# Optimization experiments

Hardware: AMD Instinct MI355X
Metric: run time of the kernel (lower is better)

## Reference

```python
import jax, jax.numpy as jnp
import numpy as np

B, C, H, W = 16, 5, 512, 512


def setup_inputs() -> dict:
    key = jax.random.key(0)
    k1, k2 = jax.random.split(key)
    y_pred = jax.random.normal(k1, (B, C, H, W), dtype=jnp.float32)
    y_true = jax.random.randint(k2, (B, H, W), 0, C, dtype=jnp.int64)
    return {"y_pred": y_pred, "y_true": y_true}


def reference(y_pred, y_true):
    # softmax over class dim
    probs = jax.nn.softmax(y_pred, axis=1)  # (B, C, H, W)
    # adjacent-class differences: diff[k-1] = p[k] - p[k-1], k = 1..C-1
    diff = probs[:, 1:] - probs[:, :-1]  # (B, C-1, H, W)
    c = y_pred.shape[1]
    k = jnp.arange(1, c).reshape(1, c - 1, 1, 1)  # class index k of diff
    t = y_true[:, None, :, :]  # true class per pixel
    # for k <= t: relu(p[k-1]-p[k]) = relu(-diff); for k > t: relu(diff)
    pen = jnp.where(k <= t, jax.nn.relu(-diff), jax.nn.relu(diff))
    # sum over k per pixel, then mean over all B*H*W pixels
    total = pen.sum()
    n_pix = y_pred.shape[0] * y_pred.shape[2] * y_pred.shape[3]
    return total / n_pix
```

## Files before the change

kernel.cpp:

```cpp
#include <hip/hip_runtime.h>

constexpr int Bn   = 16;
constexpr int Cn   = 5;
constexpr int HW   = 512 * 512;
constexpr int HW4  = HW / 4;
constexpr int NVEC = Bn * HW / 4;
constexpr int NBLK = 2048;
constexpr float SCALE = 1.0f / (float)(Bn * HW);

__device__ __forceinline__ float block_reduce_256(float v) {
    #pragma unroll
    for (int off = 32; off > 0; off >>= 1)
        v += __shfl_down(v, off, 64);
    __shared__ float s[4];
    const int lane = threadIdx.x & 63;
    const int wid  = threadIdx.x >> 6;
    if (lane == 0) s[wid] = v;
    __syncthreads();
    if (threadIdx.x == 0) v = (s[0] + s[1]) + (s[2] + s[3]);
    return v;
}

__device__ __forceinline__ float pixel_pen(float l0, float l1, float l2, float l3,
                                           float l4, int t) {
    float m  = fmaxf(fmaxf(fmaxf(l0, l1), fmaxf(l2, l3)), l4);
    float e0 = __expf(l0 - m);
    float e1 = __expf(l1 - m);
    float e2 = __expf(l2 - m);
    float e3 = __expf(l3 - m);
    float e4 = __expf(l4 - m);
    float S  = ((e0 + e1) + (e2 + e3)) + e4;
    float d1 = e1 - e0;
    float d2 = e2 - e1;
    float d3 = e3 - e2;
    float d4 = e4 - e3;
    float pen = 0.0f;
    pen += (t >= 1) ? fmaxf(-d1, 0.0f) : fmaxf(d1, 0.0f);
    pen += (t >= 2) ? fmaxf(-d2, 0.0f) : fmaxf(d2, 0.0f);
    pen += (t >= 3) ? fmaxf(-d3, 0.0f) : fmaxf(d3, 0.0f);
    pen += (t >= 4) ? fmaxf(-d4, 0.0f) : fmaxf(d4, 0.0f);
    return pen / S;
}

__global__ void __launch_bounds__(256)
o2_loss_partial(const float4* __restrict__ pred,
                const int4*  __restrict__ lab,
                float* __restrict__ partial) {
    float acc = 0.0f;
    const int stride = gridDim.x * 256;
    for (int v = blockIdx.x * 256 + threadIdx.x; v < NVEC; v += stride) {
        const int b   = v >> 16;
        const int hw4 = v & (HW4 - 1);
        const float4* base = pred + (size_t)b * (Cn * HW4) + hw4;
        float4 x0 = base[0 * HW4];
        float4 x1 = base[1 * HW4];
        float4 x2 = base[2 * HW4];
        float4 x3 = base[3 * HW4];
        float4 x4 = base[4 * HW4];
        int4   t  = lab[v];
        acc += pixel_pen(x0.x, x1.x, x2.x, x3.x, x4.x, t.x);
        acc += pixel_pen(x0.y, x1.y, x2.y, x3.y, x4.y, t.y);
        acc += pixel_pen(x0.z, x1.z, x2.z, x3.z, x4.z, t.z);
        acc += pixel_pen(x0.w, x1.w, x2.w, x3.w, x4.w, t.w);
    }
    acc = block_reduce_256(acc);
    if (threadIdx.x == 0) partial[blockIdx.x] = acc;
}

__global__ void __launch_bounds__(256)
o2_loss_finalize(const float* __restrict__ partial, float* __restrict__ out) {
    float v = 0.0f;
    for (int i = threadIdx.x; i < NBLK; i += 256)
        v += partial[i];
    v = block_reduce_256(v);
    if (threadIdx.x == 0) out[0] = v * SCALE;
}

extern "C" void kernel_launch(void* const* d_in, const int* in_sizes, int n_in,
                              void* d_out, int out_size, void* d_ws, size_t ws_size,
                              hipStream_t stream) {
    const float4* pred = (const float4*)d_in[0];
    const int4*   lab  = (const int4*)d_in[1];
    float* partial = (float*)d_ws;
    float* out     = (float*)d_out;

    o2_loss_partial<<<NBLK, 256, 0, stream>>>(pred, lab, partial);
    o2_loss_finalize<<<1, 256, 0, stream>>>(partial, out);
}
```

Measured before the change: 25.02 us.

## Fuse final reduction into main kernel via last-block atomic counter

```diff
diff --git a/kernel.cpp b/kernel.cpp
--- a/kernel.cpp
+++ b/kernel.cpp
@@ -1,11 +1,13 @@
 #include <hip/hip_runtime.h>
 
-constexpr int Bn   = 16;
-constexpr int Cn   = 5;
-constexpr int HW   = 512 * 512;
-constexpr int HW4  = HW / 4;
-constexpr int NVEC = Bn * HW / 4;
-constexpr int NBLK = 2048;
+constexpr int Bn      = 16;
+constexpr int Cn      = 5;
+constexpr int HW      = 512 * 512;
+constexpr int HW4     = HW / 4;
+constexpr int NVEC    = Bn * HW / 4;
+constexpr int NBLK    = 2048;
+constexpr int THREADS = 256;
+constexpr int STRIDE  = NBLK * THREADS;
 constexpr float SCALE = 1.0f / (float)(Bn * HW);
 
 __device__ __forceinline__ float block_reduce_256(float v) {
@@ -42,38 +44,59 @@
     return pen / S;
 }
 
-__global__ void __launch_bounds__(256)
-o2_loss_partial(const float4* __restrict__ pred,
-                const int4*  __restrict__ lab,
-                float* __restrict__ partial) {
-    float acc = 0.0f;
-    const int stride = gridDim.x * 256;
-    for (int v = blockIdx.x * 256 + threadIdx.x; v < NVEC; v += stride) {
-        const int b   = v >> 16;
-        const int hw4 = v & (HW4 - 1);
-        const float4* base = pred + (size_t)b * (Cn * HW4) + hw4;
-        float4 x0 = base[0 * HW4];
-        float4 x1 = base[1 * HW4];
-        float4 x2 = base[2 * HW4];
-        float4 x3 = base[3 * HW4];
-        float4 x4 = base[4 * HW4];
-        int4   t  = lab[v];
-        acc += pixel_pen(x0.x, x1.x, x2.x, x3.x, x4.x, t.x);
-        acc += pixel_pen(x0.y, x1.y, x2.y, x3.y, x4.y, t.y);
-        acc += pixel_pen(x0.z, x1.z, x2.z, x3.z, x4.z, t.z);
-        acc += pixel_pen(x0.w, x1.w, x2.w, x3.w, x4.w, t.w);
-    }
-    acc = block_reduce_256(acc);
-    if (threadIdx.x == 0) partial[blockIdx.x] = acc;
+__device__ __forceinline__ float group_pen(float4 x0, float4 x1, float4 x2,
+                                           float4 x3, float4 x4, int4 t) {
+    float a = 0.0f;
+    a += pixel_pen(x0.x, x1.x, x2.x, x3.x, x4.x, t.x);
+    a += pixel_pen(x0.y, x1.y, x2.y, x3.y, x4.y, t.y);
+    a += pixel_pen(x0.z, x1.z, x2.z, x3.z, x4.z, t.z);
+    a += pixel_pen(x0.w, x1.w, x2.w, x3.w, x4.w, t.w);
+    return a;
 }
 
 __global__ void __launch_bounds__(256)
-o2_loss_finalize(const float* __restrict__ partial, float* __restrict__ out) {
-    float v = 0.0f;
-    for (int i = threadIdx.x; i < NBLK; i += 256)
-        v += partial[i];
-    v = block_reduce_256(v);
-    if (threadIdx.x == 0) out[0] = v * SCALE;
+o2_loss_fused(const float4* __restrict__ pred,
+              const int4*  __restrict__ lab,
+              float* __restrict__ partial,
+              unsigned* __restrict__ cnt,
+              float* __restrict__ out) {
+    const int tid = threadIdx.x;
+    const int v0  = blockIdx.x * THREADS + tid;
+    const int b0  = v0 >> 16;
+    const int h0  = v0 & (HW4 - 1);
+    const float4* p0 = pred + (size_t)b0 * (Cn * HW4) + h0;
+    const float4* p1 = p0 + 8 * (Cn * HW4);
+
+    float4 a0 = p0[0 * HW4], a1 = p0[1 * HW4], a2 = p0[2 * HW4],
+           a3 = p0[3 * HW4], a4 = p0[4 * HW4];
+    float4 b0v = p1[0 * HW4], b1v = p1[1 * HW4], b2v = p1[2 * HW4],
+           b3v = p1[3 * HW4], b4v = p1[4 * HW4];
+    int4 t0 = lab[v0];
+    int4 t1 = lab[v0 + STRIDE];
+
+    float acc = group_pen(a0, a1, a2, a3, a4, t0)
+              + group_pen(b0v, b1v, b2v, b3v, b4v, t1);
+
+    float bsum = block_reduce_256(acc);
+
+    __shared__ int is_last;
+    if (tid == 0) {
+        __hip_atomic_store(&partial[blockIdx.x], bsum,
+                           __ATOMIC_RELAXED, __HIP_MEMORY_SCOPE_AGENT);
+        unsigned old = __hip_atomic_fetch_add(cnt, 1u,
+                           __ATOMIC_ACQ_REL, __HIP_MEMORY_SCOPE_AGENT);
+        is_last = ((old & (NBLK - 1)) == (NBLK - 1)) ? 1 : 0;
+    }
+    __syncthreads();
+
+    if (is_last) {
+        float v = 0.0f;
+        for (int i = tid; i < NBLK; i += THREADS)
+            v += __hip_atomic_load(&partial[i],
+                                   __ATOMIC_RELAXED, __HIP_MEMORY_SCOPE_AGENT);
+        v = block_reduce_256(v);
+        if (tid == 0) out[0] = v * SCALE;
+    }
 }
 
 extern "C" void kernel_launch(void* const* d_in, const int* in_sizes, int n_in,
@@ -81,9 +104,9 @@
                               hipStream_t stream) {
     const float4* pred = (const float4*)d_in[0];
     const int4*   lab  = (const int4*)d_in[1];
-    float* partial = (float*)d_ws;
-    float* out     = (float*)d_out;
+    float*    partial  = (float*)d_ws;
+    unsigned* cnt      = (unsigned*)((char*)d_ws + NBLK * sizeof(float));
+    float*    out      = (float*)d_out;
 
-    o2_loss_partial<<<NBLK, 256, 0, stream>>>(pred, lab, partial);
-    o2_loss_finalize<<<1, 256, 0, stream>>>(partial, out);
+    o2_loss_fused<<<NBLK, THREADS, 0, stream>>>(pred, lab, partial, cnt, out);
 }
```

After: 81.74 us. 3.27x slower.
